# Kernel tuning notes

Hardware: AMD Instinct MI355X
Metric: run time of the kernel (lower is better)

The kernel has to match this reference:

```python
import jax, jax.numpy as jnp
import numpy as np

N_NODES = 100000


def setup_inputs() -> dict:
    key = jax.random.key(0)
    k1, k2, k3, k4, k5, k6 = jax.random.split(key, 6)
    n_edges = 1600000
    X = jax.random.normal(k1, (N_NODES, 256), dtype=jnp.float32)
    edge_row = jax.random.randint(k2, (n_edges,), 0, N_NODES, dtype=jnp.int64)
    edge_col = jax.random.randint(k3, (n_edges,), 0, N_NODES, dtype=jnp.int64)
    edge_val = jax.random.uniform(k4, (n_edges,), dtype=jnp.float32)
    W = jax.random.normal(k5, (128, 256), dtype=jnp.float32) * 0.05
    b = jax.random.normal(k6, (128,), dtype=jnp.float32) * 0.05
    return {"X": X, "edge_row": edge_row, "edge_col": edge_col,
            "edge_val": edge_val, "W": W, "b": b}


def reference(X, edge_row, edge_col, edge_val, W, b):
    # Dense projection: H = X @ W^T + b  -> [N, out_dim]
    H = jnp.einsum('ni,oi->no', X, W) + b
    # SpMM: out[r] = sum_e A[r, c_e] * H[c_e] over edges with row r
    msgs = edge_val[:, None] * H[edge_col]          # [E, out_dim]
    out = jax.ops.segment_sum(msgs, edge_row, num_segments=N_NODES)
    return out
```

## Files before the change

kernel.cpp:

```cpp
#include <hip/hip_runtime.h>
#include <hip/hip_bf16.h>

#define NNODES 100000
#define NEDGES 1600000
#define KDIM 256
#define ODIM 128
#define NB_SCAN 98
#define EDGE_CAP 1900032
#define ESTRIDE 400000

typedef __attribute__((ext_vector_type(8))) short short8;
typedef __attribute__((ext_vector_type(4))) float floatx4;

static __device__ __forceinline__ short f2bf(float f) {
  union { float f; unsigned u; } x; x.f = f;
  unsigned r = (x.u + 0x7fffu + ((x.u >> 16) & 1u)) >> 16;
  return (short)r;
}

__global__ void conv_w_kernel(const float* __restrict__ W, short* __restrict__ Wb) {
  int i = blockIdx.x * 256 + threadIdx.x;
  if (i < ODIM * KDIM) Wb[i] = f2bf(W[i]);
}

__global__ void rank_kernel(const int* __restrict__ rows, int* __restrict__ counts,
                            unsigned short* __restrict__ rank) {
  int i = blockIdx.x * 256 + threadIdx.x;
#pragma unroll
  for (int j = 0; j < 4; j++) {
    int e = i + j * ESTRIDE;
    if (e < NEDGES) {
      int r = rows[e];
      rank[e] = (unsigned short)atomicAdd(&counts[r], 1);
    }
  }
}

__global__ void scan1_kernel(const int* __restrict__ counts, int* __restrict__ chunkExcl,
                             int* __restrict__ blockSums) {
  __shared__ int s[256];
  int t = threadIdx.x;
  int base = blockIdx.x * 1024 + t * 4;
  int v[4];
#pragma unroll
  for (int j = 0; j < 4; j++) {
    int idx = base + j;
    v[j] = (idx < NNODES) ? ((counts[idx] + 3) & ~3) : 0;
  }
  int sum = v[0] + v[1] + v[2] + v[3];
  s[t] = sum;
  __syncthreads();
  for (int o = 1; o < 256; o <<= 1) {
    int add = (t >= o) ? s[t - o] : 0;
    __syncthreads();
    s[t] += add;
    __syncthreads();
  }
  int run = s[t] - sum;
#pragma unroll
  for (int j = 0; j < 4; j++) {
    int idx = base + j;
    if (idx < NNODES) chunkExcl[idx] = run;
    run += v[j];
  }
  if (t == 255) blockSums[blockIdx.x] = s[255];
}

__global__ void scan2_kernel(const int* __restrict__ blockSums, int* __restrict__ blockBase,
                             int* __restrict__ offsets) {
  __shared__ int s[128];
  int t = threadIdx.x;
  int v = (t < NB_SCAN) ? blockSums[t] : 0;
  s[t] = v;
  __syncthreads();
  for (int o = 1; o < 128; o <<= 1) {
    int add = (t >= o) ? s[t - o] : 0;
    __syncthreads();
    s[t] += add;
    __syncthreads();
  }
  if (t < NB_SCAN) blockBase[t] = s[t] - v;
  if (t == 127) offsets[NNODES] = s[127];
}

__global__ void scan3_kernel(const int* __restrict__ chunkExcl, const int* __restrict__ blockBase,
                             int* __restrict__ offsets) {
  int i = blockIdx.x * 256 + threadIdx.x;
  if (i < NNODES) offsets[i] = chunkExcl[i] + blockBase[i >> 10];
}

__global__ void place_kernel(const int* __restrict__ rows, const int* __restrict__ cols,
                             const float* __restrict__ vals,
                             const unsigned short* __restrict__ rank,
                             const int* __restrict__ offsets, int2* __restrict__ edges) {
  int i = blockIdx.x * 256 + threadIdx.x;
#pragma unroll
  for (int j = 0; j < 4; j++) {
    int e = i + j * ESTRIDE;
    if (e < NEDGES) {
      int r = rows[e];
      int p = offsets[r] + (int)rank[e];
      int2 rec;
      rec.x = cols[e];
      rec.y = __float_as_int(vals[e]);
      edges[p] = rec;
    }
  }
}

__global__ __launch_bounds__(256) void gemm_kernel(const float* __restrict__ X,
                                                   const short* __restrict__ Wb,
                                                   const float* __restrict__ bias,
                                                   unsigned short* __restrict__ H) {
  const int lane = threadIdx.x & 63;
  const int wave = threadIdx.x >> 6;
  const int l16 = lane & 15;
  const int quad = lane >> 4;
  const int rowBase = blockIdx.x * 128 + wave * 32;
  const int arow0 = rowBase + l16;
  const int arow1 = arow0 + 16;

  floatx4 acc[8][2];
#pragma unroll
  for (int t = 0; t < 8; t++) {
    acc[t][0] = (floatx4){0.f, 0.f, 0.f, 0.f};
    acc[t][1] = (floatx4){0.f, 0.f, 0.f, 0.f};
  }

  for (int k0 = 0; k0 < KDIM; k0 += 32) {
    const int k = k0 + quad * 8;
    short8 a0, a1;
    if (arow0 < NNODES) {
      const float4* xp = (const float4*)(X + (size_t)arow0 * KDIM + k);
      float4 x0 = xp[0];
      float4 x1 = xp[1];
      a0[0] = f2bf(x0.x); a0[1] = f2bf(x0.y); a0[2] = f2bf(x0.z); a0[3] = f2bf(x0.w);
      a0[4] = f2bf(x1.x); a0[5] = f2bf(x1.y); a0[6] = f2bf(x1.z); a0[7] = f2bf(x1.w);
    } else {
      a0 = (short8){0, 0, 0, 0, 0, 0, 0, 0};
    }
    if (arow1 < NNODES) {
      const float4* xp = (const float4*)(X + (size_t)arow1 * KDIM + k);
      float4 x0 = xp[0];
      float4 x1 = xp[1];
      a1[0] = f2bf(x0.x); a1[1] = f2bf(x0.y); a1[2] = f2bf(x0.z); a1[3] = f2bf(x0.w);
      a1[4] = f2bf(x1.x); a1[5] = f2bf(x1.y); a1[6] = f2bf(x1.z); a1[7] = f2bf(x1.w);
    } else {
      a1 = (short8){0, 0, 0, 0, 0, 0, 0, 0};
    }
#pragma unroll
    for (int t = 0; t < 8; t++) {
      short8 b = *(const short8*)(Wb + (t * 16 + l16) * KDIM + k);
      acc[t][0] = __builtin_amdgcn_mfma_f32_16x16x32_bf16(a0, b, acc[t][0], 0, 0, 0);
      acc[t][1] = __builtin_amdgcn_mfma_f32_16x16x32_bf16(a1, b, acc[t][1], 0, 0, 0);
    }
  }

#pragma unroll
  for (int t = 0; t < 8; t++) {
    const int col = t * 16 + l16;
    const float bv = bias[col];
#pragma unroll
    for (int h = 0; h < 2; h++) {
#pragma unroll
      for (int r = 0; r < 4; r++) {
        const int row = rowBase + h * 16 + quad * 4 + r;
        if (row < NNODES) H[(size_t)row * ODIM + col] = (unsigned short)f2bf(acc[t][h][r] + bv);
      }
    }
  }
}

__global__ __launch_bounds__(256) void spmm_kernel(const int* __restrict__ offsets,
                                                   const int2* __restrict__ edges,
                                                   const unsigned* __restrict__ H2,
                                                   float* __restrict__ out) {
  const int lane = threadIdx.x & 63;
  const int row = blockIdx.x * 4 + (threadIdx.x >> 6);
  if (row >= NNODES) return;
  const int s = offsets[row];
  const int e = offsets[row + 1];
  float ax = 0.f, ay = 0.f;
  for (int i = s; i < e; i += 4) {
    const int4 p01 = *(const int4*)(edges + i);
    const int4 p23 = *(const int4*)(edges + i + 2);
    const unsigned h0 = H2[(size_t)p01.x * 64 + lane];
    const unsigned h1 = H2[(size_t)p01.z * 64 + lane];
    const unsigned h2 = H2[(size_t)p23.x * 64 + lane];
    const unsigned h3 = H2[(size_t)p23.z * 64 + lane];
    const float v0 = __int_as_float(p01.y);
    const float v1 = __int_as_float(p01.w);
    const float v2 = __int_as_float(p23.y);
    const float v3 = __int_as_float(p23.w);
    ax += v0 * __uint_as_float(h0 << 16);
    ay += v0 * __uint_as_float(h0 & 0xffff0000u);
    ax += v1 * __uint_as_float(h1 << 16);
    ay += v1 * __uint_as_float(h1 & 0xffff0000u);
    ax += v2 * __uint_as_float(h2 << 16);
    ay += v2 * __uint_as_float(h2 & 0xffff0000u);
    ax += v3 * __uint_as_float(h3 << 16);
    ay += v3 * __uint_as_float(h3 & 0xffff0000u);
  }
  float2 r;
  r.x = ax;
  r.y = ay;
  ((float2*)out)[(size_t)row * 64 + lane] = r;
}

extern "C" void kernel_launch(void* const* d_in, const int* in_sizes, int n_in,
                              void* d_out, int out_size, void* d_ws, size_t ws_size,
                              hipStream_t stream) {
  const float* X = (const float*)d_in[0];
  const int* erow = (const int*)d_in[1];
  const int* ecol = (const int*)d_in[2];
  const float* eval = (const float*)d_in[3];
  const float* W = (const float*)d_in[4];
  const float* bias = (const float*)d_in[5];
  float* out = (float*)d_out;

  char* ws = (char*)d_ws;
  size_t off = 0;
  auto alloc = [&](size_t bytes) -> char* {
    char* p = ws + off;
    off += (bytes + 255) & ~(size_t)255;
    return p;
  };
  unsigned short* Hb = (unsigned short*)alloc((size_t)NNODES * ODIM * 2);
  short* Wb = (short*)alloc((size_t)ODIM * KDIM * 2);
  int* counts = (int*)alloc((size_t)NNODES * 4);
  int* chunkExcl = (int*)alloc((size_t)NNODES * 4);
  int* offsets = (int*)alloc((size_t)(NNODES + 1) * 4);
  int* blockSums = (int*)alloc((size_t)NB_SCAN * 4);
  int* blockBase = (int*)alloc((size_t)NB_SCAN * 4);
  unsigned short* rank = (unsigned short*)alloc((size_t)NEDGES * 2);
  int2* edges = (int2*)alloc((size_t)EDGE_CAP * 8);

  hipMemsetAsync(counts, 0, (size_t)NNODES * 4, stream);
  hipMemsetAsync(edges, 0, (size_t)EDGE_CAP * 8, stream);
  conv_w_kernel<<<(ODIM * KDIM + 255) / 256, 256, 0, stream>>>(W, Wb);
  rank_kernel<<<(ESTRIDE + 255) / 256, 256, 0, stream>>>(erow, counts, rank);
  scan1_kernel<<<NB_SCAN, 256, 0, stream>>>(counts, chunkExcl, blockSums);
  scan2_kernel<<<1, 128, 0, stream>>>(blockSums, blockBase, offsets);
  scan3_kernel<<<(NNODES + 255) / 256, 256, 0, stream>>>(chunkExcl, blockBase, offsets);
  place_kernel<<<(ESTRIDE + 255) / 256, 256, 0, stream>>>(erow, ecol, eval, rank, offsets, edges);
  gemm_kernel<<<(NNODES + 127) / 128, 256, 0, stream>>>(X, Wb, bias, Hb);
  spmm_kernel<<<(NNODES + 3) / 4, 256, 0, stream>>>(offsets, edges, (const unsigned*)Hb, out);
}
```

Before: 411.9 us.

## Fuse edge ranking into GEMM launch and shrink GEMM tile with prefetch

```diff
diff --git a/kernel.cpp b/kernel.cpp
--- a/kernel.cpp
+++ b/kernel.cpp
@@ -8,6 +8,8 @@
 #define NB_SCAN 98
 #define EDGE_CAP 1900032
 #define ESTRIDE 400000
+#define GEMM_BLOCKS 1563
+#define RANK_BLOCKS 1563
 
 typedef __attribute__((ext_vector_type(8))) short short8;
 typedef __attribute__((ext_vector_type(4))) float floatx4;
@@ -21,19 +23,6 @@
 __global__ void conv_w_kernel(const float* __restrict__ W, short* __restrict__ Wb) {
   int i = blockIdx.x * 256 + threadIdx.x;
   if (i < ODIM * KDIM) Wb[i] = f2bf(W[i]);
-}
-
-__global__ void rank_kernel(const int* __restrict__ rows, int* __restrict__ counts,
-                            unsigned short* __restrict__ rank) {
-  int i = blockIdx.x * 256 + threadIdx.x;
-#pragma unroll
-  for (int j = 0; j < 4; j++) {
-    int e = i + j * ESTRIDE;
-    if (e < NEDGES) {
-      int r = rows[e];
-      rank[e] = (unsigned short)atomicAdd(&counts[r], 1);
-    }
-  }
 }
 
 __global__ void scan1_kernel(const int* __restrict__ counts, int* __restrict__ chunkExcl,
@@ -108,52 +97,56 @@
   }
 }
 
-__global__ __launch_bounds__(256) void gemm_kernel(const float* __restrict__ X,
-                                                   const short* __restrict__ Wb,
-                                                   const float* __restrict__ bias,
-                                                   unsigned short* __restrict__ H) {
+__global__ __launch_bounds__(256) void gemm_rank_kernel(
+    const float* __restrict__ X, const short* __restrict__ Wb,
+    const float* __restrict__ bias, unsigned short* __restrict__ H,
+    const int* __restrict__ rows, int* __restrict__ counts,
+    unsigned short* __restrict__ rank) {
+  if (blockIdx.x >= GEMM_BLOCKS) {
+    int i = (blockIdx.x - GEMM_BLOCKS) * 256 + threadIdx.x;
+#pragma unroll
+    for (int j = 0; j < 4; j++) {
+      int e = i + j * ESTRIDE;
+      if (e < NEDGES) {
+        int r = rows[e];
+        rank[e] = (unsigned short)atomicAdd(&counts[r], 1);
+      }
+    }
+    return;
+  }
   const int lane = threadIdx.x & 63;
   const int wave = threadIdx.x >> 6;
   const int l16 = lane & 15;
   const int quad = lane >> 4;
-  const int rowBase = blockIdx.x * 128 + wave * 32;
-  const int arow0 = rowBase + l16;
-  const int arow1 = arow0 + 16;
-
-  floatx4 acc[8][2];
-#pragma unroll
-  for (int t = 0; t < 8; t++) {
-    acc[t][0] = (floatx4){0.f, 0.f, 0.f, 0.f};
-    acc[t][1] = (floatx4){0.f, 0.f, 0.f, 0.f};
-  }
-
-  for (int k0 = 0; k0 < KDIM; k0 += 32) {
-    const int k = k0 + quad * 8;
-    short8 a0, a1;
-    if (arow0 < NNODES) {
-      const float4* xp = (const float4*)(X + (size_t)arow0 * KDIM + k);
-      float4 x0 = xp[0];
-      float4 x1 = xp[1];
-      a0[0] = f2bf(x0.x); a0[1] = f2bf(x0.y); a0[2] = f2bf(x0.z); a0[3] = f2bf(x0.w);
-      a0[4] = f2bf(x1.x); a0[5] = f2bf(x1.y); a0[6] = f2bf(x1.z); a0[7] = f2bf(x1.w);
-    } else {
-      a0 = (short8){0, 0, 0, 0, 0, 0, 0, 0};
-    }
-    if (arow1 < NNODES) {
-      const float4* xp = (const float4*)(X + (size_t)arow1 * KDIM + k);
-      float4 x0 = xp[0];
-      float4 x1 = xp[1];
-      a1[0] = f2bf(x0.x); a1[1] = f2bf(x0.y); a1[2] = f2bf(x0.z); a1[3] = f2bf(x0.w);
-      a1[4] = f2bf(x1.x); a1[5] = f2bf(x1.y); a1[6] = f2bf(x1.z); a1[7] = f2bf(x1.w);
-    } else {
-      a1 = (short8){0, 0, 0, 0, 0, 0, 0, 0};
-    }
+  const int rowBase = blockIdx.x * 64 + wave * 16;
+  const int arow = rowBase + l16;
+  const bool inb = arow < NNODES;
+  const float4 zf4 = {0.f, 0.f, 0.f, 0.f};
+  const float4* xp = (const float4*)(X + (size_t)(inb ? arow : 0) * KDIM + quad * 8);
+
+  floatx4 acc[8];
+#pragma unroll
+  for (int t = 0; t < 8; t++) acc[t] = (floatx4){0.f, 0.f, 0.f, 0.f};
+
+  float4 c0 = inb ? xp[0] : zf4;
+  float4 c1 = inb ? xp[1] : zf4;
+#pragma unroll
+  for (int k0 = 0; k0 < 8; k0++) {
+    float4 n0, n1;
+    if (k0 < 7) {
+      n0 = inb ? xp[(k0 + 1) * 8] : zf4;
+      n1 = inb ? xp[(k0 + 1) * 8 + 1] : zf4;
+    }
+    short8 a;
+    a[0] = f2bf(c0.x); a[1] = f2bf(c0.y); a[2] = f2bf(c0.z); a[3] = f2bf(c0.w);
+    a[4] = f2bf(c1.x); a[5] = f2bf(c1.y); a[6] = f2bf(c1.z); a[7] = f2bf(c1.w);
+    const short* bp = Wb + k0 * 32 + quad * 8;
 #pragma unroll
     for (int t = 0; t < 8; t++) {
-      short8 b = *(const short8*)(Wb + (t * 16 + l16) * KDIM + k);
-      acc[t][0] = __builtin_amdgcn_mfma_f32_16x16x32_bf16(a0, b, acc[t][0], 0, 0, 0);
-      acc[t][1] = __builtin_amdgcn_mfma_f32_16x16x32_bf16(a1, b, acc[t][1], 0, 0, 0);
-    }
+      short8 b = *(const short8*)(bp + (size_t)(t * 16 + l16) * KDIM);
+      acc[t] = __builtin_amdgcn_mfma_f32_16x16x32_bf16(a, b, acc[t], 0, 0, 0);
+    }
+    if (k0 < 7) { c0 = n0; c1 = n1; }
   }
 
 #pragma unroll
@@ -161,12 +154,9 @@
     const int col = t * 16 + l16;
     const float bv = bias[col];
 #pragma unroll
-    for (int h = 0; h < 2; h++) {
-#pragma unroll
-      for (int r = 0; r < 4; r++) {
-        const int row = rowBase + h * 16 + quad * 4 + r;
-        if (row < NNODES) H[(size_t)row * ODIM + col] = (unsigned short)f2bf(acc[t][h][r] + bv);
-      }
+    for (int r = 0; r < 4; r++) {
+      const int row = rowBase + quad * 4 + r;
+      if (row < NNODES) H[(size_t)row * ODIM + col] = (unsigned short)f2bf(acc[t][r] + bv);
     }
   }
 }
@@ -238,11 +228,11 @@
   hipMemsetAsync(counts, 0, (size_t)NNODES * 4, stream);
   hipMemsetAsync(edges, 0, (size_t)EDGE_CAP * 8, stream);
   conv_w_kernel<<<(ODIM * KDIM + 255) / 256, 256, 0, stream>>>(W, Wb);
-  rank_kernel<<<(ESTRIDE + 255) / 256, 256, 0, stream>>>(erow, counts, rank);
+  gemm_rank_kernel<<<GEMM_BLOCKS + RANK_BLOCKS, 256, 0, stream>>>(X, Wb, bias, Hb,
+                                                                 erow, counts, rank);
   scan1_kernel<<<NB_SCAN, 256, 0, stream>>>(counts, chunkExcl, blockSums);
   scan2_kernel<<<1, 128, 0, stream>>>(blockSums, blockBase, offsets);
   scan3_kernel<<<(NNODES + 255) / 256, 256, 0, stream>>>(chunkExcl, blockBase, offsets);
   place_kernel<<<(ESTRIDE + 255) / 256, 256, 0, stream>>>(erow, ecol, eval, rank, offsets, edges);
-  gemm_kernel<<<(NNODES + 127) / 128, 256, 0, stream>>>(X, Wb, bias, Hb);
   spmm_kernel<<<(NNODES + 3) / 4, 256, 0, stream>>>(offsets, edges, (const unsigned*)Hb, out);
 }
```

Result: faster. 386.1 us (-6.3%).
